# Optimization experiments

Hardware: AMD Instinct MI355X
Metric: run time of the kernel (lower is better)

The kernel has to match this reference:

```python
import jax, jax.numpy as jnp
import numpy as np

N_CELLS, D_IN, D_HID, D_OUT, MLP_W = 16384, 512, 1024, 512, 128
N_FACTIONS, SYNC, DEBATE = 8, 0.15, 0.15


def setup_inputs() -> dict:
    key = jax.random.key(0)
    ks = jax.random.split(key, 20)
    s = 0.05
    inp = {
        "x": jax.random.normal(ks[0], (1, D_IN), jnp.float32),
        "hiddens": jax.random.normal(ks[1], (N_CELLS, D_HID), jnp.float32) * 0.1,
        "wealth_norm": jax.random.uniform(ks[2], (N_CELLS,), jnp.float32, 0.5, 1.5),
        "Wa1": jax.random.normal(ks[3], (D_IN + D_HID, MLP_W), jnp.float32) * s,
        "ba1": jax.random.normal(ks[4], (MLP_W,), jnp.float32) * s,
        "Wa2": jax.random.normal(ks[5], (MLP_W, D_OUT), jnp.float32) * s,
        "ba2": jax.random.normal(ks[6], (D_OUT,), jnp.float32) * s,
        "Wg1": jax.random.normal(ks[7], (D_IN + D_HID, MLP_W), jnp.float32) * s,
        "bg1": jax.random.normal(ks[8], (MLP_W,), jnp.float32) * s,
        "Wg2": jax.random.normal(ks[9], (MLP_W, D_OUT), jnp.float32) * s,
        "bg2": jax.random.normal(ks[10], (D_OUT,), jnp.float32) * s,
        "W_ih": jax.random.normal(ks[11], (D_OUT + 1, 3 * D_HID), jnp.float32) * s,
        "W_hh": jax.random.normal(ks[12], (D_HID, 3 * D_HID), jnp.float32) * s,
        "b_ih": jax.random.normal(ks[13], (3 * D_HID,), jnp.float32) * s,
        "b_hh": jax.random.normal(ks[14], (3 * D_HID,), jnp.float32) * s,
        "Wo": jax.random.normal(ks[15], (D_OUT, D_IN), jnp.float32) * s,
        "bo": jax.random.normal(ks[16], (D_IN,), jnp.float32) * s,
        "positions": jax.random.randint(ks[17], (N_CELLS,), 0, 3, jnp.int32) - 1,
        "step": 10,
    }
    return inp


def _gru_cell(mem, h, W_ih, W_hh, b_ih, b_hh):
    # torch.nn.GRUCell math, gate order r, z, n
    gi = mem @ W_ih + b_ih            # [N, 3H]
    gh = h @ W_hh + b_hh              # [N, 3H]
    gi_r, gi_z, gi_n = jnp.split(gi, 3, axis=-1)
    gh_r, gh_z, gh_n = jnp.split(gh, 3, axis=-1)
    r = jax.nn.sigmoid(gi_r + gh_r)
    z = jax.nn.sigmoid(gi_z + gh_z)
    n = jnp.tanh(gi_n + r * gh_n)
    return (1.0 - z) * n + z * h


def _group_sync(h, mask):
    cnt = jnp.sum(mask)
    m = mask[:, None].astype(h.dtype)
    mean = jnp.sum(h * m, axis=0) / jnp.maximum(cnt, 1).astype(h.dtype)
    blended = 0.9 * h + 0.1 * mean
    return jnp.where((mask[:, None]) & (cnt >= 2), blended, h)


def _faction_sync_debate(h, step):
    n = h.shape[0]
    n_f = min(N_FACTIONS, n // 2)
    if n_f < 2:
        return h
    fs = n // n_f
    hf = h[: n_f * fs].reshape(n_f, fs, -1)
    fmean = hf.mean(axis=1, keepdims=True)                    # [n_f, 1, H]
    hf = (1.0 - SYNC) * hf + SYNC * fmean
    if step > 5:
        global_op = hf.mean(axis=1).mean(axis=0)              # [H]
        dc = max(1, fs // 4)
        head = (1.0 - DEBATE) * hf[:, :dc] + DEBATE * global_op
        hf = jnp.concatenate([head, hf[:, dc:]], axis=1)
    out = hf.reshape(n_f * fs, -1)
    if n_f * fs < n:
        out = jnp.concatenate([out, h[n_f * fs:]], axis=0)
    return out


def reference(x, hiddens, wealth_norm, Wa1, ba1, Wa2, ba2, Wg1, bg1, Wg2, bg2,
              W_ih, W_hh, b_ih, b_hh, Wo, bo, positions, step):
    n = hiddens.shape[0]
    xb = jnp.broadcast_to(x, (n, x.shape[-1]))                # same x for every cell
    combined = jnp.concatenate([xb, hiddens], axis=-1)        # [N, D_in+D_hid]
    a = jax.nn.relu(combined @ Wa1 + ba1) @ Wa2 + ba2
    g = jax.nn.relu(combined @ Wg1 + bg1) @ Wg2 + bg2
    output = a - g                                            # [N, D_out]
    tension = jnp.mean(output ** 2, axis=-1, keepdims=True)   # [N, 1]
    mem_input = jax.lax.stop_gradient(jnp.concatenate([output, tension], axis=-1))
    new_h = _gru_cell(mem_input, hiddens, W_ih, W_hh, b_ih, b_hh)
    mod = 0.9 + 0.1 * jnp.clip(wealth_norm, 0.1, 2.0)
    new_h = jnp.clip(new_h * mod[:, None], -10.0, 10.0)
    new_h = jax.lax.stop_gradient(new_h)                      # original detaches state
    new_h = _group_sync(new_h, positions > 0)
    new_h = _group_sync(new_h, positions < 0)
    new_h = _faction_sync_debate(new_h, step)
    # tension weights come from .item() in torch -> constants
    weights = jax.nn.softmax(jax.lax.stop_gradient(tension[:, 0]))
    combined_out = weights @ output                           # [D_out]
    pred = (combined_out @ Wo + bo)[None, :]                  # [1, D_in]
    avg_tension = jnp.mean(tension)
    return pred, avg_tension, new_h
```

## Files before the change

kernel.cpp:

```cpp
#include <hip/hip_runtime.h>
#include <stdint.h>

typedef unsigned short u16;
typedef __bf16 bf16x8 __attribute__((ext_vector_type(8)));
typedef float f32x4 __attribute__((ext_vector_type(4)));


__device__ __forceinline__ float bf2f(unsigned u) { return __uint_as_float(u << 16); }
__device__ __forceinline__ u16 f2bf(float f) {
  unsigned x = __float_as_uint(f);
  unsigned r = x + 0x7fffu + ((x >> 16) & 1u);
  return (u16)(r >> 16);
}
__device__ __forceinline__ unsigned pack2(float a, float b) {
  return (unsigned)f2bf(a) | ((unsigned)f2bf(b) << 16);
}
__device__ __forceinline__ float sigm(float x) { return 1.f / (1.f + __expf(-x)); }
__device__ __forceinline__ float fast_tanh(float x) {
  float e = __expf(2.f * x);
  return 1.f - 2.f / (e + 1.f);
}

#define AS1(p) ((const __attribute__((address_space(1))) void*)(p))
#define AS3(p) ((__attribute__((address_space(3))) void*)(p))

#define NC 16384

__device__ __forceinline__ void packT_body(
    const float* __restrict__ src, int sld, int srow0,
    u16* __restrict__ dst, int dld, int drow0, int koff,
    int remapThresh, int remapAdd, float sgn, int bx, int by,
    float (*tile)[65], int t) {
  const int k0 = by * 64, c0 = bx * 64;
  const int tx = t & 15, ty = t >> 4;
#pragma unroll
  for (int p = 0; p < 4; ++p) {
    int r = ty + p * 16;
    float4 v = *reinterpret_cast<const float4*>(&src[(size_t)(srow0 + k0 + r) * sld + c0 + tx * 4]);
    tile[tx * 4 + 0][r] = v.x;
    tile[tx * 4 + 1][r] = v.y;
    tile[tx * 4 + 2][r] = v.z;
    tile[tx * 4 + 3][r] = v.w;
  }
  __syncthreads();
  const int cl = t >> 2;
  const int kb = (t & 3) * 16;
  int col = c0 + cl;
  int row = drow0 + col + ((col >= remapThresh) ? remapAdd : 0);
  union { u16 o[16]; uint4 v[2]; } u;
#pragma unroll
  for (int e = 0; e < 16; ++e) u.o[e] = f2bf(sgn * tile[cl][kb + e]);
  uint4* d = reinterpret_cast<uint4*>(&dst[(size_t)row * dld + koff + k0 + kb]);
  d[0] = u.v[0]; d[1] = u.v[1];
}

__global__ __launch_bounds__(256) void prep_kernel(
    const float* __restrict__ hid, u16* __restrict__ hidc,
    const float* __restrict__ W_ih, const float* __restrict__ W_hh, u16* __restrict__ WgruT,
    const float* __restrict__ Wa1, const float* __restrict__ Wg1, u16* __restrict__ W1catT,
    const float* __restrict__ Wa2, const float* __restrict__ Wg2, u16* __restrict__ W2catT,
    const float* __restrict__ x, const float* __restrict__ ba1, const float* __restrict__ bg1,
    float* __restrict__ bias1, const float* __restrict__ ba2, const float* __restrict__ bg2,
    float* __restrict__ bias2, const int* __restrict__ positions, int* __restrict__ counts) {
  __shared__ float tile[64][65];
  int b = blockIdx.x, t = threadIdx.x;
  if (b < 16384) {
    int i = b * 256 + t;
    float4 v = ((const float4*)hid)[i];
    uint2 o; o.x = pack2(v.x, v.y); o.y = pack2(v.z, v.w);
    ((uint2*)hidc)[i] = o;
    return;
  }
  b -= 16384;
  if (b < 768) {
    packT_body(W_hh, 3072, 0, WgruT, 1536, 0, 512, 2048, 1024, 1.f, b % 48, b / 48, tile, t);
    return;
  }
  b -= 768;
  if (b < 384) {
    packT_body(W_ih, 3072, 0, WgruT, 1536, 0, 0, 1 << 30, 0, 1.f, b % 48, b / 48, tile, t);
    return;
  }
  b -= 384;
  if (b < 32) { packT_body(Wa1, 128, 512, W1catT, 1024, 0, 0, 1 << 30, 0, 1.f, b % 2, b / 2, tile, t); return; }
  b -= 32;
  if (b < 32) { packT_body(Wg1, 128, 512, W1catT, 1024, 128, 0, 1 << 30, 0, 1.f, b % 2, b / 2, tile, t); return; }
  b -= 32;
  if (b < 16) { packT_body(Wa2, 512, 0, W2catT, 256, 0, 0, 1 << 30, 0, 1.f, b % 8, b / 8, tile, t); return; }
  b -= 16;
  if (b < 16) { packT_body(Wg2, 512, 0, W2catT, 256, 0, 128, 1 << 30, 0, -1.f, b % 8, b / 8, tile, t); return; }
  b -= 16;
  if (b < 8) {
    const float* W = (t < 128) ? Wa1 : Wg1;
    int cc = t & 127;
    float acc = 0.f;
    int k0 = b * 64;
    for (int k = k0; k < k0 + 64; ++k) acc += x[k] * W[(size_t)k * 128 + cc];
    if (b == 0) acc += (t < 128) ? ba1[cc] : bg1[cc];
    atomicAdd(&bias1[t], acc);
    return;
  }
  b -= 8;
  if (b < 2) { int n = b * 256 + t; bias2[n] = ba2[n] - bg2[n]; return; }
  b -= 2;
  {
    int i = b * 256 + t;
    int p = positions[i], f = i >> 11;
    if (p > 0) atomicAdd(&counts[f * 2], 1);
    else if (p < 0) atomicAdd(&counts[f * 2 + 1], 1);
  }
}

__global__ __launch_bounds__(256) void gemm_bt(
    const u16* __restrict__ A, int lda,
    const u16* __restrict__ Bt, int ldb,
    u16* __restrict__ C, int ldc,
    const float* __restrict__ bias, int epi, int K,
    float* __restrict__ tension) {
  __shared__ __align__(16) u16 As[3][128 * 32];
  __shared__ __align__(16) u16 Bs[3][128 * 32];
  const int tid = threadIdx.x;
  const int m0 = blockIdx.x * 128;
  const int n0 = blockIdx.y * 128;
  f32x4 acc[4][4] = {};
  const int lane = tid & 63;
  const int w = tid >> 6;
  const int mw = (w & 1) * 64, nw = (w >> 1) * 64;
  const int fr = lane & 15;
  const int q = lane >> 4;
  const int ar0 = tid >> 2;
  const int ag = ((tid & 3) ^ ((ar0 >> 1) & 3)) * 8;

  const u16* aB0 = A + (size_t)(m0 + ar0) * lda + ag;
  const u16* aB1 = A + (size_t)(m0 + ar0 + 64) * lda + ag;
  const u16* bB0 = Bt + (size_t)(n0 + ar0) * ldb + ag;
  const u16* bB1 = Bt + (size_t)(n0 + ar0 + 64) * ldb + ag;

  auto stage = [&](int kk, int buf) {
    __builtin_amdgcn_global_load_lds(AS1(aB0 + kk), AS3(&As[buf][tid * 8]), 16, 0, 0);
    __builtin_amdgcn_global_load_lds(AS1(aB1 + kk), AS3(&As[buf][(tid + 256) * 8]), 16, 0, 0);
    __builtin_amdgcn_global_load_lds(AS1(bB0 + kk), AS3(&Bs[buf][tid * 8]), 16, 0, 0);
    __builtin_amdgcn_global_load_lds(AS1(bB1 + kk), AS3(&Bs[buf][(tid + 256) * 8]), 16, 0, 0);
  };

  const int NT = K >> 5;
  stage(0, 0);
  stage(32, 1);
  int cur = 0, nxt = 1, nx2 = 2;
#pragma unroll 1
  for (int t = 0; t < NT; ++t) {
    if (t + 2 < NT) stage((t + 2) * 32, nx2);
    const int rem = NT - 1 - t;
    if (rem >= 2)      asm volatile("s_waitcnt vmcnt(8)" ::: "memory");
    else if (rem == 1) asm volatile("s_waitcnt vmcnt(4)" ::: "memory");
    else               asm volatile("s_waitcnt vmcnt(0)" ::: "memory");
    __builtin_amdgcn_s_barrier();
    asm volatile("" ::: "memory");
    bf16x8 af[4], bfv[4];
#pragma unroll
    for (int mt = 0; mt < 4; ++mt) {
      int r = mw + mt * 16 + fr;
      af[mt] = *reinterpret_cast<const bf16x8*>(&As[cur][r * 32 + ((q ^ ((r >> 1) & 3)) * 8)]);
    }
#pragma unroll
    for (int nt = 0; nt < 4; ++nt) {
      int r = nw + nt * 16 + fr;
      bfv[nt] = *reinterpret_cast<const bf16x8*>(&Bs[cur][r * 32 + ((q ^ ((r >> 1) & 3)) * 8)]);
    }
    __builtin_amdgcn_s_setprio(1);
#pragma unroll
    for (int mt = 0; mt < 4; ++mt)
#pragma unroll
      for (int nt = 0; nt < 4; ++nt)
        acc[mt][nt] = __builtin_amdgcn_mfma_f32_16x16x32_bf16(af[mt], bfv[nt], acc[mt][nt], 0, 0, 0);
    __builtin_amdgcn_s_setprio(0);
    asm volatile("s_waitcnt lgkmcnt(0)" ::: "memory");
    __builtin_amdgcn_s_barrier();
    int tmp = cur; cur = nxt; nxt = nx2; nx2 = tmp;
  }
  const int rq = q * 4;
#pragma unroll
  for (int mt = 0; mt < 4; ++mt) {
    float srow[4] = {0.f, 0.f, 0.f, 0.f};
#pragma unroll
    for (int nt = 0; nt < 4; ++nt) {
      int col = n0 + nw + nt * 16 + fr;
      f32x4 v = acc[mt][nt];
#pragma unroll
      for (int r = 0; r < 4; ++r) {
        int row = m0 + mw + mt * 16 + rq + r;
        float val = v[r] + bias[col];
        if (epi == 1) val = val > 0.f ? val : 0.f;
        else srow[r] += val * val;
        C[(size_t)row * ldc + col] = f2bf(val);
      }
    }
    if (epi == 3) {
#pragma unroll
      for (int r = 0; r < 4; ++r) {
        float s = srow[r];
        s += __shfl_xor(s, 1, 16); s += __shfl_xor(s, 2, 16);
        s += __shfl_xor(s, 4, 16); s += __shfl_xor(s, 8, 16);
        if (fr == 0) atomicAdd(&tension[m0 + mw + mt * 16 + rq + r], s);
      }
    }
  }
}

__global__ __launch_bounds__(512, 4) void gemm_gru(
    const u16* __restrict__ outbf, const u16* __restrict__ hidc,
    const u16* __restrict__ WgruT,
    const float* __restrict__ W_ihf, const float* __restrict__ bihf,
    const float* __restrict__ bhhf, const float* __restrict__ wealthf,
    const float* __restrict__ tension, u16* __restrict__ hpre) {
  __shared__ __align__(16) u16 As[3][128 * 32];
  __shared__ __align__(16) u16 Bs[3][3][64 * 32];
  const int tid = threadIdx.x;
  const int m0 = blockIdx.x * 128;
  const int j0 = blockIdx.y * 64;
  f32x4 acc[4][2][2] = {};
  const int lane = tid & 63;
  const int w = tid >> 6;
  const int mw = (w & 3) * 32, nw = (w >> 2) * 32;
  const int fr = lane & 15;
  const int q = lane >> 4;
  const int arow = tid >> 2;
  const int ag = ((tid & 3) ^ ((arow >> 1) & 3)) * 8;
  const int ct = tid & 255;
  const int brow = ct >> 2;
  const int bg = ((ct & 3) ^ ((brow >> 1) & 3)) * 8;
  const int bsel = tid >> 8;

  const u16* aB0 = outbf + (size_t)(m0 + arow) * 512 + ag;
  const u16* aB1 = hidc + (size_t)(m0 + arow) * 1024 + ag;
  const u16* bBR = WgruT + (size_t)((bsel ? 1024 : 0) + j0 + brow) * 1536 + bg;

  auto stage = [&](int s, int buf) {
    const int p = s >= 16;
    const u16* ap = p ? (aB1 + (s - 16) * 32) : (aB0 + s * 32);
    __builtin_amdgcn_global_load_lds(AS1(ap), AS3(&As[buf][tid * 8]), 16, 0, 0);
    const int kk = s * 32;
    if (bsel == 0) {
      __builtin_amdgcn_global_load_lds(AS1(bBR + kk), AS3(&Bs[buf][0][ct * 8]), 16, 0, 0);
      __builtin_amdgcn_global_load_lds(
          AS1(bBR + (size_t)(2048 * 1536 + (p ? 1024 * 1536 : 0) + kk)),
          AS3(&Bs[buf][2][ct * 8]), 16, 0, 0);
    } else {
      __builtin_amdgcn_global_load_lds(AS1(bBR + kk), AS3(&Bs[buf][1][ct * 8]), 16, 0, 0);
    }
  };

  stage(0, 0);
  stage(1, 1);
  int cur = 0, nxt = 1, nx2 = 2;

#define GRU_STEP(T, REG3)                                                                     \
  {                                                                                           \
    if ((T) < 46) {                                                                           \
      stage((T) + 2, nx2);                                                                    \
      if (bsel == 0) asm volatile("s_waitcnt vmcnt(6)" ::: "memory");                         \
      else           asm volatile("s_waitcnt vmcnt(4)" ::: "memory");                         \
    } else if ((T) == 46) {                                                                   \
      if (bsel == 0) asm volatile("s_waitcnt vmcnt(3)" ::: "memory");                         \
      else           asm volatile("s_waitcnt vmcnt(2)" ::: "memory");                         \
    } else {                                                                                  \
      asm volatile("s_waitcnt vmcnt(0)" ::: "memory");                                        \
    }                                                                                         \
    __builtin_amdgcn_s_barrier();                                                             \
    asm volatile("" ::: "memory");                                                            \
    bf16x8 af[2], b0v[2], b1v[2], b2v[2];                                                     \
    _Pragma("unroll")                                                                         \
    for (int mt = 0; mt < 2; ++mt) {                                                          \
      int r = mw + mt * 16 + fr;                                                              \
      af[mt] = *reinterpret_cast<const bf16x8*>(&As[cur][r * 32 + ((q ^ ((r >> 1) & 3)) * 8)]);\
    }                                                                                         \
    _Pragma("unroll")                                                                         \
    for (int nt = 0; nt < 2; ++nt) {                                                          \
      int r = nw + nt * 16 + fr;                                                              \
      int ss = (q ^ ((r >> 1) & 3)) * 8;                                                      \
      b0v[nt] = *reinterpret_cast<const bf16x8*>(&Bs[cur][0][r * 32 + ss]);                   \
      b1v[nt] = *reinterpret_cast<const bf16x8*>(&Bs[cur][1][r * 32 + ss]);                   \
      b2v[nt] = *reinterpret_cast<const bf16x8*>(&Bs[cur][2][r * 32 + ss]);                   \
    }                                                                                         \
    __builtin_amdgcn_s_setprio(1);                                                            \
    _Pragma("unroll")                                                                         \
    for (int mt = 0; mt < 2; ++mt)                                                            \
      _Pragma("unroll")                                                                       \
      for (int nt = 0; nt < 2; ++nt) {                                                        \
        acc[0][mt][nt] = __builtin_amdgcn_mfma_f32_16x16x32_bf16(af[mt], b0v[nt], acc[0][mt][nt], 0, 0, 0); \
        acc[1][mt][nt] = __builtin_amdgcn_mfma_f32_16x16x32_bf16(af[mt], b1v[nt], acc[1][mt][nt], 0, 0, 0); \
        acc[REG3][mt][nt] = __builtin_amdgcn_mfma_f32_16x16x32_bf16(af[mt], b2v[nt], acc[REG3][mt][nt], 0, 0, 0); \
      }                                                                                       \
    __builtin_amdgcn_s_setprio(0);                                                            \
    asm volatile("s_waitcnt lgkmcnt(0)" ::: "memory");                                        \
    __builtin_amdgcn_s_barrier();                                                             \
    int tmp = cur; cur = nxt; nxt = nx2; nx2 = tmp;                                           \
  }

#pragma unroll 1
  for (int t = 0; t < 16; ++t) GRU_STEP(t, 2)
#pragma unroll 1
  for (int t = 16; t < 48; ++t) GRU_STEP(t, 3)
#undef GRU_STEP

  const int rq = q * 4;
  const float* wt = W_ihf + (size_t)512 * 3072;
  float wtr[2], wtz[2], wtn[2], bir[2], biz[2], bin_[2], bhr_[2], bhz_[2], bhn_[2];
#pragma unroll
  for (int nt = 0; nt < 2; ++nt) {
    int j = j0 + nw + nt * 16 + fr;
    wtr[nt] = wt[j]; wtz[nt] = wt[1024 + j]; wtn[nt] = wt[2048 + j];
    bir[nt] = bihf[j]; biz[nt] = bihf[1024 + j]; bin_[nt] = bihf[2048 + j];
    bhr_[nt] = bhhf[j]; bhz_[nt] = bhhf[1024 + j]; bhn_[nt] = bhhf[2048 + j];
  }
#pragma unroll
  for (int mt = 0; mt < 2; ++mt) {
#pragma unroll
    for (int rr = 0; rr < 4; ++rr) {
      int row = m0 + mw + mt * 16 + rq + rr;
      float tv = tension[row] * (1.f / 512.f);
      float wl = fminf(fmaxf(wealthf[row], 0.1f), 2.0f);
      float mod = 0.9f + 0.1f * wl;
#pragma unroll
      for (int nt = 0; nt < 2; ++nt) {
        int j = j0 + nw + nt * 16 + fr;
        float r = sigm(acc[0][mt][nt][rr] + tv * wtr[nt] + bir[nt] + bhr_[nt]);
        float z = sigm(acc[1][mt][nt][rr] + tv * wtz[nt] + biz[nt] + bhz_[nt]);
        float n = fast_tanh(acc[2][mt][nt][rr] + tv * wtn[nt] + bin_[nt]
                            + r * (acc[3][mt][nt][rr] + bhn_[nt]));
        float h = bf2f(hidc[(size_t)row * 1024 + j]);
        float h2 = (1.f - z) * n + z * h;
        h2 = fminf(fmaxf(h2 * mod, -10.f), 10.f);
        hpre[(size_t)row * 1024 + j] = f2bf(h2);
      }
    }
  }
}

__global__ void stats_kernel(const u16* __restrict__ hpre, const int* __restrict__ positions,
                             float* __restrict__ fsums) {
  int cc = blockIdx.x, f = blockIdx.y, z = blockIdx.z, t = threadIdx.x;
  int col = cc * 128 + (t & 127);
  int half = t >> 7;
  float st = 0, sp = 0, sm = 0;
  for (int it = 0; it < 128; ++it) {
    int row = (f << 11) + ((z * 128 + it) << 1) + half;
    int p = positions[row];
    float v = bf2f(hpre[(size_t)row * 1024 + col]);
    st += v;
    if (p > 0) sp += v;
    if (p < 0) sm += v;
  }
  atomicAdd(&fsums[(f * 3 + 0) * 1024 + col], st);
  atomicAdd(&fsums[(f * 3 + 1) * 1024 + col], sp);
  atomicAdd(&fsums[(f * 3 + 2) * 1024 + col], sm);
}

__global__ void derive_kernel(const float* __restrict__ fsums, const int* __restrict__ counts,
                              float* __restrict__ mean1, float* __restrict__ mean2,
                              float* __restrict__ fmean, float* __restrict__ gop,
                              float* __restrict__ scal) {
  int c = threadIdx.x;
  int cnt1 = 0, cnt2 = 0, cf1[8], cf2[8];
#pragma unroll
  for (int f = 0; f < 8; ++f) {
    cf1[f] = counts[f * 2]; cf2[f] = counts[f * 2 + 1];
    cnt1 += cf1[f]; cnt2 += cf2[f];
  }
  float s1 = 0, s2 = 0;
#pragma unroll
  for (int f = 0; f < 8; ++f) { s1 += fsums[(f * 3 + 1) * 1024 + c]; s2 += fsums[(f * 3 + 2) * 1024 + c]; }
  float m1 = s1 / (float)(cnt1 > 1 ? cnt1 : 1);
  float m2 = s2 / (float)(cnt2 > 1 ? cnt2 : 1);
  float a1 = (cnt1 >= 2) ? 0.1f : 0.f;
  float a2 = (cnt2 >= 2) ? 0.1f : 0.f;
  float g = 0;
#pragma unroll
  for (int f = 0; f < 8; ++f) {
    float fm = (fsums[(f * 3) * 1024 + c]
                + a1 * ((float)cf1[f] * m1 - fsums[(f * 3 + 1) * 1024 + c])
                + a2 * ((float)cf2[f] * m2 - fsums[(f * 3 + 2) * 1024 + c])) * (1.f / 2048.f);
    fmean[f * 1024 + c] = fm;
    g += fm;
  }
  gop[c] = g * 0.125f;
  mean1[c] = m1; mean2[c] = m2;
  if (c == 0) { scal[0] = a1; scal[1] = a2; }
}

__global__ void finalize_kernel(const u16* __restrict__ hpre, const int* __restrict__ positions,
                                const int* __restrict__ step, const float* __restrict__ mean1,
                                const float* __restrict__ mean2, const float* __restrict__ fmean,
                                const float* __restrict__ gop, const float* __restrict__ scal,
                                float* __restrict__ out) {
  int row = blockIdx.x, t = threadIdx.x;
  int p = positions[row];
  float w1 = (p > 0) ? scal[0] : 0.f;
  float w2 = (p < 0) ? scal[1] : 0.f;
  int f = row >> 11, q = row & 2047;
  bool deb = (step[0] > 5) && (q < 512);
  const u16* hrow = hpre + (size_t)row * 1024;
  const float* fmp = fmean + f * 1024;
  float* orow = out + 513 + (size_t)row * 1024;
#pragma unroll
  for (int e = 0; e < 8; ++e) {
    int c = e * 128 + t;
    float h = bf2f(hrow[c]);
    float hgs = h + w1 * (mean1[c] - h) + w2 * (mean2[c] - h);
    float hfs = 0.85f * hgs + 0.15f * fmp[c];
    orow[c] = deb ? (0.85f * hfs + 0.15f * gop[c]) : hfs;
  }
}

__global__ void softmax_kernel(const float* __restrict__ tension, float* __restrict__ weights,
                               float* __restrict__ out) {
  __shared__ float red[1024];
  int t = threadIdx.x;
  float tv[16], mx = -1e30f, sumt = 0.f;
#pragma unroll
  for (int k = 0; k < 16; ++k) {
    tv[k] = tension[t + k * 1024] * (1.f / 512.f);
    mx = fmaxf(mx, tv[k]); sumt += tv[k];
  }
  red[t] = mx; __syncthreads();
  for (int s = 512; s > 0; s >>= 1) { if (t < s) red[t] = fmaxf(red[t], red[t + s]); __syncthreads(); }
  float m = red[0]; __syncthreads();
  red[t] = sumt; __syncthreads();
  for (int s = 512; s > 0; s >>= 1) { if (t < s) red[t] += red[t + s]; __syncthreads(); }
  float tot = red[0]; __syncthreads();
  float ev[16], se = 0.f;
#pragma unroll
  for (int k = 0; k < 16; ++k) { ev[k] = __expf(tv[k] - m); se += ev[k]; }
  red[t] = se; __syncthreads();
  for (int s = 512; s > 0; s >>= 1) { if (t < s) red[t] += red[t + s]; __syncthreads(); }
  float invS = 1.f / red[0];
#pragma unroll
  for (int k = 0; k < 16; ++k) weights[t + k * 1024] = ev[k] * invS;
  if (t == 0) out[512] = tot * (1.f / 16384.f);
}

__global__ void wsum_kernel(const float* __restrict__ weights, const u16* __restrict__ outbf,
                            float* __restrict__ co) {
  int b = blockIdx.x, t = threadIdx.x;
  int c = t * 2;
  float a0 = 0.f, a1 = 0.f;
  int i0 = b * 128;
  for (int i = i0; i < i0 + 128; ++i) {
    float w = weights[i];
    unsigned v = *reinterpret_cast<const unsigned*>(outbf + (size_t)i * 512 + c);
    a0 += w * bf2f(v & 0xffff);
    a1 += w * bf2f(v >> 16);
  }
  atomicAdd(&co[c], a0);
  atomicAdd(&co[c + 1], a1);
}

__global__ void pred_kernel(const float* __restrict__ co, const float* __restrict__ Wof,
                            const float* __restrict__ bof, float* __restrict__ out) {
  __shared__ float cs[512];
  int t = threadIdx.x, n = blockIdx.x * 256 + t;
  cs[t] = co[t]; cs[t + 256] = co[t + 256];
  __syncthreads();
  float acc = bof[n];
  for (int ck = 0; ck < 512; ++ck) acc += cs[ck] * Wof[(size_t)ck * 512 + n];
  out[n] = acc;
}

extern "C" void kernel_launch(void* const* d_in, const int* in_sizes, int n_in,
                              void* d_out, int out_size, void* d_ws, size_t ws_size,
                              hipStream_t stream) {
  const float* x      = (const float*)d_in[0];
  const float* hid    = (const float*)d_in[1];
  const float* wealth = (const float*)d_in[2];
  const float* Wa1    = (const float*)d_in[3];
  const float* ba1    = (const float*)d_in[4];
  const float* Wa2    = (const float*)d_in[5];
  const float* ba2    = (const float*)d_in[6];
  const float* Wg1    = (const float*)d_in[7];
  const float* bg1    = (const float*)d_in[8];
  const float* Wg2    = (const float*)d_in[9];
  const float* bg2    = (const float*)d_in[10];
  const float* W_ih   = (const float*)d_in[11];
  const float* W_hh   = (const float*)d_in[12];
  const float* b_ih   = (const float*)d_in[13];
  const float* b_hh   = (const float*)d_in[14];
  const float* Wo     = (const float*)d_in[15];
  const float* bo     = (const float*)d_in[16];
  const int* positions= (const int*)d_in[17];
  const int* step     = (const int*)d_in[18];
  float* out = (float*)d_out;

  char* w = (char*)d_ws;
  size_t off = 0;
  auto alloc = [&](size_t bytes) { void* p = w + off; off += (bytes + 255) & ~(size_t)255; return p; };
  u16*   hidc    = (u16*)  alloc((size_t)NC * 1024 * 2);
  u16*   outbf   = (u16*)  alloc((size_t)NC * 512 * 2);
  u16*   hpre    = (u16*)  alloc((size_t)NC * 1024 * 2);
  u16*   WgruT   = (u16*)  alloc((size_t)4096 * 1536 * 2);
  u16*   W1catT  = (u16*)  alloc((size_t)256 * 1024 * 2);
  u16*   W2catT  = (u16*)  alloc((size_t)512 * 256 * 2);
  u16*   t1      = (u16*)  alloc((size_t)NC * 256 * 2);
  float* bias1   = (float*)alloc(256 * 4);
  float* co      = (float*)alloc(512 * 4);
  int*   counts  = (int*)  alloc(16 * 4);
  float* fsums   = (float*)alloc(8 * 3 * 1024 * 4);
  float* tension = (float*)alloc(NC * 4);
  float* bias2   = (float*)alloc(512 * 4);
  float* weights = (float*)alloc(NC * 4);
  float* mean1   = (float*)alloc(1024 * 4);
  float* mean2   = (float*)alloc(1024 * 4);
  float* gop     = (float*)alloc(1024 * 4);
  float* fmean   = (float*)alloc(8 * 1024 * 4);
  float* scal    = (float*)alloc(8 * 4);

  hipMemsetAsync(bias1, 0, 1024 + 2048 + 256 + 98304 + 65536, stream);

  prep_kernel<<<17706, 256, 0, stream>>>(hid, hidc, W_ih, W_hh, WgruT,
                                         Wa1, Wg1, W1catT, Wa2, Wg2, W2catT,
                                         x, ba1, bg1, bias1, ba2, bg2, bias2,
                                         positions, counts);

  gemm_bt<<<dim3(128, 2), 256, 0, stream>>>(hidc, 1024, W1catT, 1024, t1, 256,
                                            bias1, 1, 1024, nullptr);
  gemm_bt<<<dim3(128, 4), 256, 0, stream>>>(t1, 256, W2catT, 256, outbf, 512,
                                            bias2, 3, 256, tension);

  gemm_gru<<<dim3(128, 16), 512, 0, stream>>>(outbf, hidc, WgruT, W_ih, b_ih, b_hh,
                                              wealth, tension, hpre);

  stats_kernel<<<dim3(8, 8, 8), 256, 0, stream>>>(hpre, positions, fsums);
  derive_kernel<<<1, 1024, 0, stream>>>(fsums, counts, mean1, mean2, fmean, gop, scal);
  finalize_kernel<<<NC, 128, 0, stream>>>(hpre, positions, step, mean1, mean2, fmean, gop,
                                          scal, out);

  softmax_kernel<<<1, 1024, 0, stream>>>(tension, weights, out);
  wsum_kernel<<<128, 256, 0, stream>>>(weights, outbf, co);
  pred_kernel<<<2, 256, 0, stream>>>(co, Wo, bo, out);

  (void)in_sizes; (void)n_in; (void)out_size; (void)ws_size;
}
```

Before: 598.8 us.

## Enlarge GRU GEMM tile to 128x128 with K=64 double-buffered pipeline

Reworks the fused GRU GEMM so each block computes 128 rows by 128 hidden columns across all three gates, with a K-step of 64 and a two-buffer LDS pipeline replacing the three-buffer K=32 one. The next stage is issued mid-step, after the second half-K fragments are read, so loads overlap the second batch of MFMAs, and the swizzle changes to an 8-way XOR. The larger tile halves how often the A operand is reloaded per output column, raises MFMA work per barrier, and halves the grid. The cost is more LDS (about 128KB), more accumulator registers and lower occupancy (launch bounds 2 instead of 4).

```diff
diff --git a/kernel.cpp b/kernel.cpp
--- a/kernel.cpp
+++ b/kernel.cpp
@@ -207,114 +207,135 @@
   }
 }
 
-__global__ __launch_bounds__(512, 4) void gemm_gru(
+__global__ __launch_bounds__(512, 2) void gemm_gru(
     const u16* __restrict__ outbf, const u16* __restrict__ hidc,
     const u16* __restrict__ WgruT,
     const float* __restrict__ W_ihf, const float* __restrict__ bihf,
     const float* __restrict__ bhhf, const float* __restrict__ wealthf,
     const float* __restrict__ tension, u16* __restrict__ hpre) {
-  __shared__ __align__(16) u16 As[3][128 * 32];
-  __shared__ __align__(16) u16 Bs[3][3][64 * 32];
+  __shared__ __align__(16) u16 As[2][128 * 64];
+  __shared__ __align__(16) u16 Bs[2][3][128 * 64];
   const int tid = threadIdx.x;
   const int m0 = blockIdx.x * 128;
-  const int j0 = blockIdx.y * 64;
-  f32x4 acc[4][2][2] = {};
+  const int j0 = blockIdx.y * 128;
+  f32x4 acc[4][4][2] = {};
   const int lane = tid & 63;
   const int w = tid >> 6;
-  const int mw = (w & 3) * 32, nw = (w >> 2) * 32;
+  const int mw = (w & 1) * 64, jw = (w >> 1) * 32;
   const int fr = lane & 15;
   const int q = lane >> 4;
-  const int arow = tid >> 2;
-  const int ag = ((tid & 3) ^ ((arow >> 1) & 3)) * 8;
-  const int ct = tid & 255;
-  const int brow = ct >> 2;
-  const int bg = ((ct & 3) ^ ((brow >> 1) & 3)) * 8;
-  const int bsel = tid >> 8;
-
-  const u16* aB0 = outbf + (size_t)(m0 + arow) * 512 + ag;
-  const u16* aB1 = hidc + (size_t)(m0 + arow) * 1024 + ag;
-  const u16* bBR = WgruT + (size_t)((bsel ? 1024 : 0) + j0 + brow) * 1536 + bg;
-
-  auto stage = [&](int s, int buf) {
-    const int p = s >= 16;
-    const u16* ap = p ? (aB1 + (s - 16) * 32) : (aB0 + s * 32);
-    __builtin_amdgcn_global_load_lds(AS1(ap), AS3(&As[buf][tid * 8]), 16, 0, 0);
-    const int kk = s * 32;
-    if (bsel == 0) {
-      __builtin_amdgcn_global_load_lds(AS1(bBR + kk), AS3(&Bs[buf][0][ct * 8]), 16, 0, 0);
-      __builtin_amdgcn_global_load_lds(
-          AS1(bBR + (size_t)(2048 * 1536 + (p ? 1024 * 1536 : 0) + kk)),
-          AS3(&Bs[buf][2][ct * 8]), 16, 0, 0);
-    } else {
-      __builtin_amdgcn_global_load_lds(AS1(bBR + kk), AS3(&Bs[buf][1][ct * 8]), 16, 0, 0);
-    }
-  };
-
-  stage(0, 0);
-  stage(1, 1);
-  int cur = 0, nxt = 1, nx2 = 2;
-
-#define GRU_STEP(T, REG3)                                                                     \
-  {                                                                                           \
-    if ((T) < 46) {                                                                           \
-      stage((T) + 2, nx2);                                                                    \
-      if (bsel == 0) asm volatile("s_waitcnt vmcnt(6)" ::: "memory");                         \
-      else           asm volatile("s_waitcnt vmcnt(4)" ::: "memory");                         \
-    } else if ((T) == 46) {                                                                   \
-      if (bsel == 0) asm volatile("s_waitcnt vmcnt(3)" ::: "memory");                         \
-      else           asm volatile("s_waitcnt vmcnt(2)" ::: "memory");                         \
-    } else {                                                                                  \
-      asm volatile("s_waitcnt vmcnt(0)" ::: "memory");                                        \
-    }                                                                                         \
-    __builtin_amdgcn_s_barrier();                                                             \
-    asm volatile("" ::: "memory");                                                            \
-    bf16x8 af[2], b0v[2], b1v[2], b2v[2];                                                     \
-    _Pragma("unroll")                                                                         \
-    for (int mt = 0; mt < 2; ++mt) {                                                          \
-      int r = mw + mt * 16 + fr;                                                              \
-      af[mt] = *reinterpret_cast<const bf16x8*>(&As[cur][r * 32 + ((q ^ ((r >> 1) & 3)) * 8)]);\
-    }                                                                                         \
-    _Pragma("unroll")                                                                         \
-    for (int nt = 0; nt < 2; ++nt) {                                                          \
-      int r = nw + nt * 16 + fr;                                                              \
-      int ss = (q ^ ((r >> 1) & 3)) * 8;                                                      \
-      b0v[nt] = *reinterpret_cast<const bf16x8*>(&Bs[cur][0][r * 32 + ss]);                   \
-      b1v[nt] = *reinterpret_cast<const bf16x8*>(&Bs[cur][1][r * 32 + ss]);                   \
-      b2v[nt] = *reinterpret_cast<const bf16x8*>(&Bs[cur][2][r * 32 + ss]);                   \
-    }                                                                                         \
-    __builtin_amdgcn_s_setprio(1);                                                            \
-    _Pragma("unroll")                                                                         \
-    for (int mt = 0; mt < 2; ++mt)                                                            \
-      _Pragma("unroll")                                                                       \
-      for (int nt = 0; nt < 2; ++nt) {                                                        \
-        acc[0][mt][nt] = __builtin_amdgcn_mfma_f32_16x16x32_bf16(af[mt], b0v[nt], acc[0][mt][nt], 0, 0, 0); \
-        acc[1][mt][nt] = __builtin_amdgcn_mfma_f32_16x16x32_bf16(af[mt], b1v[nt], acc[1][mt][nt], 0, 0, 0); \
-        acc[REG3][mt][nt] = __builtin_amdgcn_mfma_f32_16x16x32_bf16(af[mt], b2v[nt], acc[REG3][mt][nt], 0, 0, 0); \
-      }                                                                                       \
-    __builtin_amdgcn_s_setprio(0);                                                            \
-    asm volatile("s_waitcnt lgkmcnt(0)" ::: "memory");                                        \
-    __builtin_amdgcn_s_barrier();                                                             \
-    int tmp = cur; cur = nxt; nxt = nx2; nx2 = tmp;                                           \
-  }
-
+  const int rowl = tid >> 3;
+  const int koffT = ((tid & 7) ^ (rowl & 7)) * 8;
+  const size_t aOutB = (size_t)(m0 + rowl) * 512 + koffT;
+  const size_t aHidB = (size_t)(m0 + rowl) * 1024 + koffT;
+  const size_t bB    = (size_t)(j0 + rowl) * 1536 + koffT;
+  const int f7 = fr & 7;
+  const int sk0 = (q ^ f7) * 8;
+  const int sk1 = ((4 + q) ^ f7) * 8;
+
+#define STAGE(S, BUF)                                                                              \
+  {                                                                                                \
+    const size_t kO = (size_t)(S) * 64;                                                            \
+    if ((S) < 8) {                                                                                 \
+      __builtin_amdgcn_global_load_lds(AS1(outbf + aOutB + kO), AS3(&As[BUF][tid * 8]), 16, 0, 0); \
+      __builtin_amdgcn_global_load_lds(AS1(outbf + aOutB + (size_t)64 * 512 + kO),                 \
+                                       AS3(&As[BUF][4096 + tid * 8]), 16, 0, 0);                   \
+    } else {                                                                                       \
+      const size_t kO1 = (size_t)((S) - 8) * 64;                                                   \
+      __builtin_amdgcn_global_load_lds(AS1(hidc + aHidB + kO1), AS3(&As[BUF][tid * 8]), 16, 0, 0); \
+      __builtin_amdgcn_global_load_lds(AS1(hidc + aHidB + (size_t)64 * 1024 + kO1),                \
+                                       AS3(&As[BUF][4096 + tid * 8]), 16, 0, 0);                   \
+    }                                                                                              \
+    const u16* bp = WgruT + bB + kO;                                                               \
+    __builtin_amdgcn_global_load_lds(AS1(bp), AS3(&Bs[BUF][0][tid * 8]), 16, 0, 0);                \
+    __builtin_amdgcn_global_load_lds(AS1(bp + (size_t)64 * 1536),                                  \
+                                     AS3(&Bs[BUF][0][4096 + tid * 8]), 16, 0, 0);                  \
+    __builtin_amdgcn_global_load_lds(AS1(bp + (size_t)1024 * 1536),                                \
+                                     AS3(&Bs[BUF][1][tid * 8]), 16, 0, 0);                         \
+    __builtin_amdgcn_global_load_lds(AS1(bp + (size_t)1088 * 1536),                                \
+                                     AS3(&Bs[BUF][1][4096 + tid * 8]), 16, 0, 0);                  \
+    const size_t nOff = ((S) < 8 ? (size_t)2048 * 1536 : (size_t)3072 * 1536);                     \
+    __builtin_amdgcn_global_load_lds(AS1(bp + nOff), AS3(&Bs[BUF][2][tid * 8]), 16, 0, 0);         \
+    __builtin_amdgcn_global_load_lds(AS1(bp + nOff + (size_t)64 * 1536),                           \
+                                     AS3(&Bs[BUF][2][4096 + tid * 8]), 16, 0, 0);                  \
+  }
+
+#define GRU_STEP(T, REG3, CUR)                                                                     \
+  {                                                                                                \
+    bf16x8 af0[4], b00[2], b10[2], b20[2];                                                         \
+    _Pragma("unroll") for (int mt = 0; mt < 4; ++mt)                                               \
+        af0[mt] = *reinterpret_cast<const bf16x8*>(&As[CUR][(mw + mt * 16 + fr) * 64 + sk0]);      \
+    _Pragma("unroll") for (int nt = 0; nt < 2; ++nt) {                                             \
+      int rj = (jw + nt * 16 + fr) * 64 + sk0;                                                     \
+      b00[nt] = *reinterpret_cast<const bf16x8*>(&Bs[CUR][0][rj]);                                 \
+      b10[nt] = *reinterpret_cast<const bf16x8*>(&Bs[CUR][1][rj]);                                 \
+      b20[nt] = *reinterpret_cast<const bf16x8*>(&Bs[CUR][2][rj]);                                 \
+    }                                                                                              \
+    __builtin_amdgcn_s_setprio(1);                                                                 \
+    _Pragma("unroll") for (int mt = 0; mt < 4; ++mt)                                               \
+        _Pragma("unroll") for (int nt = 0; nt < 2; ++nt) {                                         \
+      acc[0][mt][nt] = __builtin_amdgcn_mfma_f32_16x16x32_bf16(af0[mt], b00[nt], acc[0][mt][nt], 0, 0, 0); \
+      acc[1][mt][nt] = __builtin_amdgcn_mfma_f32_16x16x32_bf16(af0[mt], b10[nt], acc[1][mt][nt], 0, 0, 0); \
+      acc[REG3][mt][nt] = __builtin_amdgcn_mfma_f32_16x16x32_bf16(af0[mt], b20[nt], acc[REG3][mt][nt], 0, 0, 0); \
+    }                                                                                              \
+    __builtin_amdgcn_s_setprio(0);                                                                 \
+    bf16x8 af1[4], b01[2], b11[2], b21[2];                                                         \
+    _Pragma("unroll") for (int mt = 0; mt < 4; ++mt)                                               \
+        af1[mt] = *reinterpret_cast<const bf16x8*>(&As[CUR][(mw + mt * 16 + fr) * 64 + sk1]);      \
+    _Pragma("unroll") for (int nt = 0; nt < 2; ++nt) {                                             \
+      int rj = (jw + nt * 16 + fr) * 64 + sk1;                                                     \
+      b01[nt] = *reinterpret_cast<const bf16x8*>(&Bs[CUR][0][rj]);                                 \
+      b11[nt] = *reinterpret_cast<const bf16x8*>(&Bs[CUR][1][rj]);                                 \
+      b21[nt] = *reinterpret_cast<const bf16x8*>(&Bs[CUR][2][rj]);                                 \
+    }                                                                                              \
+    asm volatile("s_waitcnt lgkmcnt(0)" ::: "memory");                                             \
+    __builtin_amdgcn_s_barrier();                                                                  \
+    asm volatile("" ::: "memory");                                                                 \
+    if ((T) + 2 < 24) { STAGE((T) + 2, CUR) }                                                      \
+    __builtin_amdgcn_s_setprio(1);                                                                 \
+    _Pragma("unroll") for (int mt = 0; mt < 4; ++mt)                                               \
+        _Pragma("unroll") for (int nt = 0; nt < 2; ++nt) {                                         \
+      acc[0][mt][nt] = __builtin_amdgcn_mfma_f32_16x16x32_bf16(af1[mt], b01[nt], acc[0][mt][nt], 0, 0, 0); \
+      acc[1][mt][nt] = __builtin_amdgcn_mfma_f32_16x16x32_bf16(af1[mt], b11[nt], acc[1][mt][nt], 0, 0, 0); \
+      acc[REG3][mt][nt] = __builtin_amdgcn_mfma_f32_16x16x32_bf16(af1[mt], b21[nt], acc[REG3][mt][nt], 0, 0, 0); \
+    }                                                                                              \
+    __builtin_amdgcn_s_setprio(0);                                                                 \
+    if ((T) + 2 < 24)      { asm volatile("s_waitcnt vmcnt(8)" ::: "memory"); }                    \
+    else if ((T) + 1 < 24) { asm volatile("s_waitcnt vmcnt(0)" ::: "memory"); }                    \
+    __builtin_amdgcn_s_barrier();                                                                  \
+    asm volatile("" ::: "memory");                                                                 \
+  }
+
+  STAGE(0, 0)
+  STAGE(1, 1)
+  asm volatile("s_waitcnt vmcnt(8)" ::: "memory");
+  __builtin_amdgcn_s_barrier();
+  asm volatile("" ::: "memory");
 #pragma unroll 1
-  for (int t = 0; t < 16; ++t) GRU_STEP(t, 2)
+  for (int T = 0; T < 8; T += 2) {
+    GRU_STEP(T, 2, 0)
+    GRU_STEP(T + 1, 2, 1)
+  }
 #pragma unroll 1
-  for (int t = 16; t < 48; ++t) GRU_STEP(t, 3)
+  for (int T = 8; T < 24; T += 2) {
+    GRU_STEP(T, 3, 0)
+    GRU_STEP(T + 1, 3, 1)
+  }
 #undef GRU_STEP
+#undef STAGE
 
   const int rq = q * 4;
   const float* wt = W_ihf + (size_t)512 * 3072;
   float wtr[2], wtz[2], wtn[2], bir[2], biz[2], bin_[2], bhr_[2], bhz_[2], bhn_[2];
 #pragma unroll
   for (int nt = 0; nt < 2; ++nt) {
-    int j = j0 + nw + nt * 16 + fr;
+    int j = j0 + jw + nt * 16 + fr;
     wtr[nt] = wt[j]; wtz[nt] = wt[1024 + j]; wtn[nt] = wt[2048 + j];
     bir[nt] = bihf[j]; biz[nt] = bihf[1024 + j]; bin_[nt] = bihf[2048 + j];
     bhr_[nt] = bhhf[j]; bhz_[nt] = bhhf[1024 + j]; bhn_[nt] = bhhf[2048 + j];
   }
 #pragma unroll
-  for (int mt = 0; mt < 2; ++mt) {
+  for (int mt = 0; mt < 4; ++mt) {
 #pragma unroll
     for (int rr = 0; rr < 4; ++rr) {
       int row = m0 + mw + mt * 16 + rq + rr;
@@ -323,7 +344,7 @@
       float mod = 0.9f + 0.1f * wl;
 #pragma unroll
       for (int nt = 0; nt < 2; ++nt) {
-        int j = j0 + nw + nt * 16 + fr;
+        int j = j0 + jw + nt * 16 + fr;
         float r = sigm(acc[0][mt][nt][rr] + tv * wtr[nt] + bir[nt] + bhr_[nt]);
         float z = sigm(acc[1][mt][nt][rr] + tv * wtz[nt] + biz[nt] + bhz_[nt]);
         float n = fast_tanh(acc[2][mt][nt][rr] + tv * wtn[nt] + bin_[nt]
@@ -525,8 +546,8 @@
   gemm_bt<<<dim3(128, 4), 256, 0, stream>>>(t1, 256, W2catT, 256, outbf, 512,
                                             bias2, 3, 256, tension);
 
-  gemm_gru<<<dim3(128, 16), 512, 0, stream>>>(outbf, hidc, WgruT, W_ih, b_ih, b_hh,
-                                              wealth, tension, hpre);
+  gemm_gru<<<dim3(128, 8), 512, 0, stream>>>(outbf, hidc, WgruT, W_ih, b_ih, b_hh,
+                                             wealth, tension, hpre);
 
   stats_kernel<<<dim3(8, 8, 8), 256, 0, stream>>>(hpre, positions, fsums);
   derive_kernel<<<1, 1024, 0, stream>>>(fsums, counts, mean1, mean2, fmean, gop, scal);
```

After: 577.5 us. -3.6%, faster.
